# Optimization experiments

Measured on AMD Instinct MI355X. Metric: run time of the kernel, lower is better.

Reference implementation:

```python
import jax, jax.numpy as jnp
import numpy as np

BATCH, N_CHAN, N_FREQ, N_FRAMES = 4, 4, 257, 2000
N_TAPS, N_DELAY, N_ITER = 2, 1, 3
EPS = 1e-3        # eps passed to constructor (used by ISS updates / normalization / proj back)
EPS_MODEL = 1e-5  # eps_models['laplace'] used inside LaplaceModel


def setup_inputs() -> dict:
    key = jax.random.key(0)
    k1, k2 = jax.random.split(key)
    shape = (BATCH, N_CHAN, N_FREQ, N_FRAMES)
    return {
        "X_real": jax.random.normal(k1, shape, dtype=jnp.float32),
        "X_imag": jax.random.normal(k2, shape, dtype=jnp.float32),
    }


def mag_sq(x):
    return jnp.square(x.real) + jnp.square(x.imag)


def divide(num, denom, eps=EPS):
    # torchiva.divide: num / clamp(denom, min=eps); denom is always real here
    return num / jnp.maximum(denom, eps)


def laplace_weights(X):
    # LaplaceModel: 1 / clamp(2*sqrt(sum_f |X|^2), min=eps), broadcast over freq
    denom = 2.0 * jnp.sqrt(jnp.sum(mag_sq(X), axis=-2, keepdims=True))
    return jnp.broadcast_to(1.0 / jnp.maximum(denom, EPS_MODEL), X.shape)


def iss_block_update_type_1(src, X, weights, eps=EPS):
    n_frames = X.shape[-1]
    norm = 1.0 / n_frames
    Xs = X[..., src, :, :]                                            # (..., f, n)
    v_num = jnp.einsum('bcfn,bcfn,bfn->bcf', weights, X, Xs.conj()) * norm
    v_denom = jnp.einsum('bcfn,bfn->bcf', weights, mag_sq(Xs)) * norm
    v = divide(v_num, v_denom, eps)                                   # complex (..., c, f)
    v_s = 1.0 - 1.0 / jnp.sqrt(jnp.maximum(v_denom[..., src, :], eps))
    return v.at[..., src, :].set(v_s.astype(v.dtype))


def iss_block_update_type_2(src, tap, X, X_bar, weights, eps=EPS):
    n_frames = X.shape[-1]
    norm = 1.0 / n_frames
    Xst = X_bar[..., src, :, tap, :]                                  # (..., f, n)
    v_num = jnp.einsum('bcfn,bcfn,bfn->bcf', weights, X, Xst.conj()) * norm
    v_denom = jnp.einsum('bcfn,bfn->bcf', weights, mag_sq(Xst)) * norm
    return divide(v_num, v_denom, eps)


def iss_updates(X, X_bar, W, weights, eps=EPS):
    n_chan = X.shape[-3]
    n_taps = X_bar.shape[-2]
    # sequential rank-1 source updates
    for src in range(n_chan):
        v = iss_block_update_type_1(src, X, weights, eps)
        X = X - jnp.einsum('bcf,bfn->bcfn', v, X[..., src, :, :])
        W = W - jnp.einsum('bcf,bfd->bcfd', v, W[..., src, :, :])
    # sequential rank-1 tap (dereverberation) updates
    for src in range(n_chan):
        for tap in range(n_taps):
            v = iss_block_update_type_2(src, tap, X, X_bar, weights, eps)
            X = X - jnp.einsum('bcf,bfn->bcfn', v, X_bar[..., src, :, tap, :])
    return X, W


def projection_back(Y, W, eps=1e-6):
    n_chan = Y.shape[-3]
    eye = jnp.eye(n_chan, dtype=W.dtype)
    e1 = eye[:, :1]                                                   # ref_mic = 0, shape (c, 1)
    WT = jnp.swapaxes(jnp.swapaxes(W, -3, -2), -2, -1)                # (..., f, d, c)
    a = jnp.linalg.solve(WT + eps * eye, e1)                          # (..., f, c, 1)
    a = jnp.swapaxes(a, -3, -2)                                       # (..., c, f, 1)
    return Y * a


def _forward(X_real, X_imag):
    X = jax.lax.complex(X_real, X_imag)                               # (b, c, f, n)
    batch_shape = X.shape[:-3]
    n_chan, n_freq, n_frames = X.shape[-3:]

    # hankel view of zero-padded signal -> delayed frames X_bar (b, c, f, taps, n)
    P = N_TAPS + N_DELAY
    X_pad = jnp.pad(X, [(0, 0)] * (X.ndim - 1) + [(P, 0)])
    X_bar = jnp.stack([X_pad[..., t:t + n_frames] for t in range(N_TAPS)], axis=-2)

    # demixing filters initialized to identity: W[b, c, f, d] = I[c, d]
    eye = jnp.eye(n_chan, dtype=X.dtype)
    W = jnp.broadcast_to(eye[:, None, :], batch_shape + (n_chan, n_freq, n_chan))

    for _ in range(N_ITER):
        weights = laplace_weights(X)
        g = jnp.maximum(jnp.mean(mag_sq(X), axis=(-2, -1), keepdims=True), EPS)
        g_sqrt = jnp.sqrt(g)
        X = divide(X, g_sqrt, EPS)
        W = divide(W, g_sqrt, EPS)
        weights = weights * g
        X, W = iss_updates(X, X_bar, W, weights, EPS)

    X = projection_back(X, W, eps=EPS)
    # return real/imag stacked so the output is a real float32 array
    return jnp.stack([X.real, X.imag], axis=0)


def reference(X_real, X_imag):
    return _forward(X_real, X_imag)
```

## Files before the change

### kernel.cpp

```cpp
#include <hip/hip_runtime.h>
#include <math.h>

#define NB   4
#define NC   4
#define NF   257
#define NFRM 2000
#define PLANE (NB*NC*NF*NFRM)
#define EPS  1e-3f
#define INV_FN (1.0f/514000.0f)

#define RFC  29
#define RFP  9
#define UT   512
#define UK   4

__device__ __forceinline__ float2 cmulf(float2 a, float2 b) {
  return make_float2(a.x*b.x - a.y*b.y, a.x*b.y + a.y*b.x);
}

#define DPP_STAGE(x, CTRL)                                                \
  x += __int_as_float(__builtin_amdgcn_update_dpp(                        \
        0, __float_as_int(x), CTRL, 0xf, 0xf, true))

__device__ __forceinline__ void wave_reduce12(float* acc) {
  #pragma unroll
  for (int i=0;i<12;i++) {
    float xv = acc[i];
    DPP_STAGE(xv, 0x111);
    DPP_STAGE(xv, 0x112);
    DPP_STAGE(xv, 0x114);
    DPP_STAGE(xv, 0x118);
    DPP_STAGE(xv, 0x142);
    DPP_STAGE(xv, 0x143);
    acc[i] = xv;
  }
}

__global__ __launch_bounds__(256)
void k_zero(float* __restrict__ rsum, float* __restrict__ gpart) {
  int idx = blockIdx.x*256 + threadIdx.x;
  if (idx < 32000) rsum[idx] = 0.f;
  else if (idx < 32048) gpart[idx-32000] = 0.f;
}

__global__ __launch_bounds__(256)
void k_r(const float* __restrict__ Xr, const float* __restrict__ Xi,
         float* __restrict__ rsum, float* __restrict__ gpart)
{
  const int tid = threadIdx.x;
  const int q   = blockIdx.x*256 + tid;
  const int fc  = blockIdx.y;
  const int bc  = blockIdx.z;
  float4 s4 = make_float4(0.f,0.f,0.f,0.f);
  if (q < 500) {
    const int f0 = fc*RFP;
    const int f1 = (f0+RFP < NF) ? (f0+RFP) : NF;
    const float4* r4 = (const float4*)(Xr + (size_t)(bc*NF+f0)*NFRM) + q;
    const float4* i4 = (const float4*)(Xi + (size_t)(bc*NF+f0)*NFRM) + q;
    for (int f=f0; f<f1; ++f) {
      float4 a = *r4, b2 = *i4;
      s4.x += a.x*a.x + b2.x*b2.x;
      s4.y += a.y*a.y + b2.y*b2.y;
      s4.z += a.z*a.z + b2.z*b2.z;
      s4.w += a.w*a.w + b2.w*b2.w;
      r4 += 500; i4 += 500;
    }
    float* rp = rsum + bc*NFRM + q*4;
    atomicAdd(rp+0, s4.x); atomicAdd(rp+1, s4.y);
    atomicAdd(rp+2, s4.z); atomicAdd(rp+3, s4.w);
  }
  float t = s4.x+s4.y+s4.z+s4.w;
  #pragma unroll
  for (int o=32;o;o>>=1) t += __shfl_down(t, o);
  __shared__ float wred[4];
  if ((tid & 63) == 0) wred[tid>>6] = t;
  __syncthreads();
  if (tid == 0) atomicAdd(&gpart[bc], wred[0]+wred[1]+wred[2]+wred[3]);
}

__global__ __launch_bounds__(256)
void k_w(float* __restrict__ rsum, const float* __restrict__ gpart,
         float* __restrict__ w0g)
{
  int idx = blockIdx.x*256 + threadIdx.x;
  int bc  = idx / NFRM;
  float g = fmaxf(gpart[bc]*INV_FN, EPS);
  float r = rsum[idx];
  float s = fmaxf(2.0f*sqrtf(r), 1e-5f);
  w0g[idx] = g * __builtin_amdgcn_rcpf(s);
  rsum[idx] = 0.f;
}

#define REDUCE12()                                                        \
  {                                                                       \
    wave_reduce12(acc);                                                   \
    if ((tid & 63) == 63) {                                               \
      const int wid = tid >> 6;                                           \
      *(float4*)&wpart[wid][0] = make_float4(acc[0],acc[1],acc[2],acc[3]);\
      *(float4*)&wpart[wid][4] = make_float4(acc[4],acc[5],acc[6],acc[7]);\
      *(float4*)&wpart[wid][8] = make_float4(acc[8],acc[9],acc[10],acc[11]);\
    }                                                                     \
    __syncthreads();                                                      \
    if (tid < 12) {                                                       \
      float t = 0.f;                                                      \
      _Pragma("unroll")                                                   \
      for (int w=0;w<8;w++) t += wpart[w][tid];                           \
      vredL[tid] = t;                                                     \
    }                                                                     \
    __syncthreads();                                                      \
    {                                                                     \
      float4 vv0 = *(const float4*)&vredL[0];                             \
      float4 vv1 = *(const float4*)&vredL[4];                             \
      float4 vv2 = *(const float4*)&vredL[8];                             \
      vsum[0]=vv0.x; vsum[1]=vv0.y; vsum[2] =vv0.z; vsum[3] =vv0.w;       \
      vsum[4]=vv1.x; vsum[5]=vv1.y; vsum[6] =vv1.z; vsum[7] =vv1.w;       \
      vsum[8]=vv2.x; vsum[9]=vv2.y; vsum[10]=vv2.z; vsum[11]=vv2.w;       \
    }                                                                     \
  }

template<bool FIRST, bool LAST>
__global__ __launch_bounds__(UT, 2)
void k_u(const float* Xsr, const float* Xsi,
         const float* __restrict__ Xor_, const float* __restrict__ Xoi_,
         float* Xdr, float* Xdi,
         const float* __restrict__ w0gbuf,
         const float* __restrict__ gpart,
         float2* __restrict__ Wg)
{
  __shared__ __align__(16) float wpart[8][16];
  __shared__ __align__(16) float vredL[16];
  __shared__ float2 Wl[NC][NC];
  __shared__ float2 avec[NC];

  const int tid = threadIdx.x;
  const int f = blockIdx.x;
  const int b = blockIdx.y;
  const bool valid = tid < 500;
  const int n0 = tid*UK;
  const float norm = 1.0f/(float)NFRM;

  float igs[NC];
  #pragma unroll
  for (int c=0;c<NC;c++) {
    float g = fmaxf(gpart[b*NC+c]*INV_FN, EPS);
    igs[c] = __builtin_amdgcn_rsqf(g);
  }

  float2 x[NC][UK];
  #pragma unroll
  for (int c=0;c<NC;c++) {
    #pragma unroll
    for (int k=0;k<UK;k++) x[c][k] = make_float2(0.f,0.f);
    if (valid) {
      const size_t rb = ((size_t)(b*NC+c)*NF + f)*NFRM;
      float4 r0 = *(const float4*)(Xsr + rb + n0);
      float4 i0 = *(const float4*)(Xsi + rb + n0);
      x[c][0] = make_float2(r0.x*igs[c], i0.x*igs[c]);
      x[c][1] = make_float2(r0.y*igs[c], i0.y*igs[c]);
      x[c][2] = make_float2(r0.z*igs[c], i0.z*igs[c]);
      x[c][3] = make_float2(r0.w*igs[c], i0.w*igs[c]);
    }
  }
  float w0g[NC][UK];
  #pragma unroll
  for (int c=0;c<NC;c++) {
    #pragma unroll
    for (int k=0;k<UK;k++) w0g[c][k] = 0.f;
    if (valid) {
      float4 w4 = *(const float4*)(w0gbuf + (b*NC+c)*NFRM + n0);
      w0g[c][0]=w4.x; w0g[c][1]=w4.y; w0g[c][2]=w4.z; w0g[c][3]=w4.w;
    }
  }
  if (tid < 16) {
    const int c = tid>>2, d = tid&3;
    float2 w;
    if (FIRST) w = make_float2((c==d)?1.f:0.f, 0.f);
    else       w = Wg[(size_t)(b*NF+f)*16 + tid];
    Wl[c][d] = make_float2(w.x*igs[c], w.y*igs[c]);
  }

  #pragma unroll
  for (int s=0;s<NC;s++) {
    float acc[12];
    #pragma unroll
    for (int i=0;i<12;i++) acc[i] = 0.f;
    #pragma unroll
    for (int k=0;k<UK;k++) {
      float2 xs = x[s][k];
      float m = xs.x*xs.x + xs.y*xs.y;
      #pragma unroll
      for (int c=0;c<NC;c++) {
        float2 xc = x[c][k];
        float w = w0g[c][k];
        acc[c]   += w*(xc.x*xs.x + xc.y*xs.y);
        acc[4+c] += w*(xc.y*xs.x - xc.x*xs.y);
        acc[8+c] += w*m;
      }
    }
    float vsum[12];
    REDUCE12();
    float2 v[NC];
    #pragma unroll
    for (int c=0;c<NC;c++) {
      float dn = fmaxf(vsum[8+c]*norm, EPS);
      float rc = __builtin_amdgcn_rcpf(dn) * norm;
      v[c] = make_float2(vsum[c]*rc, vsum[4+c]*rc);
    }
    v[s] = make_float2(1.0f - __builtin_amdgcn_rsqf(fmaxf(vsum[8+s]*norm, EPS)), 0.f);
    #pragma unroll
    for (int k=0;k<UK;k++) {
      float2 xs = x[s][k];
      #pragma unroll
      for (int c=0;c<NC;c++) {
        float2 xv = x[c][k];
        xv.x -= v[c].x*xs.x - v[c].y*xs.y;
        xv.y -= v[c].x*xs.y + v[c].y*xs.x;
        x[c][k] = xv;
      }
    }
    if (tid < 16) {
      const int c = tid>>2, d = tid&3;
      float2 wsd = Wl[s][d];
      float2 wv = Wl[c][d];
      wv.x -= v[c].x*wsd.x - v[c].y*wsd.y;
      wv.y -= v[c].x*wsd.y + v[c].y*wsd.x;
      Wl[c][d] = wv;
    }
  }

  float winr[8], wini[8], nxtr[8], nxti[8];
  {
    const size_t ob = ((size_t)(b*NC+0)*NF + f)*NFRM;
    float4 m1r=make_float4(0,0,0,0), m1i=m1r, p0r=m1r, p0i=m1r;
    if (valid) {
      const float* tp = Xor_ + ob + n0;
      const float* ti = Xoi_ + ob + n0;
      if (tid > 0) { m1r = *(const float4*)(tp-4); m1i = *(const float4*)(ti-4); }
      p0r = *(const float4*)tp;  p0i = *(const float4*)ti;
    }
    winr[0]=m1r.x; winr[1]=m1r.y; winr[2]=m1r.z; winr[3]=m1r.w;
    winr[4]=p0r.x; winr[5]=p0r.y; winr[6]=p0r.z; winr[7]=p0r.w;
    wini[0]=m1i.x; wini[1]=m1i.y; wini[2]=m1i.z; wini[3]=m1i.w;
    wini[4]=p0i.x; wini[5]=p0i.y; wini[6]=p0i.z; wini[7]=p0i.w;
  }
  #pragma unroll 1
  for (int s=0;s<NC;s++) {
    if (s < NC-1) {
      const size_t ob = ((size_t)(b*NC+s+1)*NF + f)*NFRM;
      float4 m1r=make_float4(0,0,0,0), m1i=m1r, p0r=m1r, p0i=m1r;
      if (valid) {
        const float* tp = Xor_ + ob + n0;
        const float* ti = Xoi_ + ob + n0;
        if (tid > 0) { m1r = *(const float4*)(tp-4); m1i = *(const float4*)(ti-4); }
        p0r = *(const float4*)tp;  p0i = *(const float4*)ti;
      }
      nxtr[0]=m1r.x; nxtr[1]=m1r.y; nxtr[2]=m1r.z; nxtr[3]=m1r.w;
      nxtr[4]=p0r.x; nxtr[5]=p0r.y; nxtr[6]=p0r.z; nxtr[7]=p0r.w;
      nxti[0]=m1i.x; nxti[1]=m1i.y; nxti[2]=m1i.z; nxti[3]=m1i.w;
      nxti[4]=p0i.x; nxti[5]=p0i.y; nxti[6]=p0i.z; nxti[7]=p0i.w;
    }
    #pragma unroll
    for (int t2=0;t2<2;t2++) {
      float acc[12];
      #pragma unroll
      for (int i=0;i<12;i++) acc[i] = 0.f;
      #pragma unroll
      for (int k=0;k<UK;k++) {
        float2 xs = make_float2(winr[k+1+t2], wini[k+1+t2]);
        float m = xs.x*xs.x + xs.y*xs.y;
        #pragma unroll
        for (int c=0;c<NC;c++) {
          float2 xc = x[c][k];
          float w = w0g[c][k];
          acc[c]   += w*(xc.x*xs.x + xc.y*xs.y);
          acc[4+c] += w*(xc.y*xs.x - xc.x*xs.y);
          acc[8+c] += w*m;
        }
      }
      float vsum[12];
      REDUCE12();
      float2 v[NC];
      #pragma unroll
      for (int c=0;c<NC;c++) {
        float dn = fmaxf(vsum[8+c]*norm, EPS);
        float rc = __builtin_amdgcn_rcpf(dn) * norm;
        v[c] = make_float2(vsum[c]*rc, vsum[4+c]*rc);
      }
      #pragma unroll
      for (int k=0;k<UK;k++) {
        float2 xs = make_float2(winr[k+1+t2], wini[k+1+t2]);
        #pragma unroll
        for (int c=0;c<NC;c++) {
          float2 xv = x[c][k];
          xv.x -= v[c].x*xs.x - v[c].y*xs.y;
          xv.y -= v[c].x*xs.y + v[c].y*xs.x;
          x[c][k] = xv;
        }
      }
    }
    #pragma unroll
    for (int j=0;j<8;j++) { winr[j]=nxtr[j]; wini[j]=nxti[j]; }
  }

  if (LAST) {
    if (tid == 0) {
      float2 A[4][4], bb[4], xv[4];
      for (int i=0;i<4;i++)
        for (int j=0;j<4;j++)
          A[i][j] = Wl[j][i];
      for (int i=0;i<4;i++) A[i][i].x += 1e-6f;
      bb[0] = make_float2(1.f,0.f);
      bb[1] = make_float2(0.f,0.f);
      bb[2] = make_float2(0.f,0.f);
      bb[3] = make_float2(0.f,0.f);
      for (int col=0; col<4; ++col) {
        int p = col;
        float best = A[col][col].x*A[col][col].x + A[col][col].y*A[col][col].y;
        for (int r=col+1;r<4;r++) {
          float m = A[r][col].x*A[r][col].x + A[r][col].y*A[r][col].y;
          if (m > best) { best = m; p = r; }
        }
        if (p != col) {
          for (int j=0;j<4;j++) { float2 ts = A[col][j]; A[col][j] = A[p][j]; A[p][j] = ts; }
          float2 ts = bb[col]; bb[col] = bb[p]; bb[p] = ts;
        }
        float2 piv = A[col][col];
        float ib = 1.0f / (piv.x*piv.x + piv.y*piv.y);
        float2 inv = make_float2(piv.x*ib, -piv.y*ib);
        for (int r=col+1;r<4;r++) {
          float2 fac = cmulf(A[r][col], inv);
          for (int j=col;j<4;j++) {
            float2 pr = cmulf(fac, A[col][j]);
            A[r][j].x -= pr.x; A[r][j].y -= pr.y;
          }
          float2 pb = cmulf(fac, bb[col]);
          bb[r].x -= pb.x; bb[r].y -= pb.y;
        }
      }
      for (int r=3;r>=0;r--) {
        float2 t = bb[r];
        for (int j=r+1;j<4;j++) {
          float2 pr = cmulf(A[r][j], xv[j]);
          t.x -= pr.x; t.y -= pr.y;
        }
        float2 d = A[r][r];
        float ib = 1.0f/(d.x*d.x + d.y*d.y);
        xv[r] = cmulf(t, make_float2(d.x*ib, -d.y*ib));
      }
      for (int c=0;c<4;c++) avec[c] = xv[c];
    }
    __syncthreads();
    if (valid) {
      #pragma unroll
      for (int c=0;c<NC;c++) {
        const size_t rb = ((size_t)(b*NC+c)*NF + f)*NFRM;
        float2 a = avec[c];
        float2 y0 = cmulf(a, x[c][0]), y1 = cmulf(a, x[c][1]);
        float2 y2 = cmulf(a, x[c][2]), y3 = cmulf(a, x[c][3]);
        *(float4*)(Xdr + rb + n0) = make_float4(y0.x,y1.x,y2.x,y3.x);
        *(float4*)(Xdi + rb + n0) = make_float4(y0.y,y1.y,y2.y,y3.y);
      }
    }
  } else {
    if (valid) {
      #pragma unroll
      for (int c=0;c<NC;c++) {
        const size_t rb = ((size_t)(b*NC+c)*NF + f)*NFRM;
        *(float4*)(Xdr + rb + n0) = make_float4(x[c][0].x,x[c][1].x,x[c][2].x,x[c][3].x);
        *(float4*)(Xdi + rb + n0) = make_float4(x[c][0].y,x[c][1].y,x[c][2].y,x[c][3].y);
      }
    }
    if (tid < 16) Wg[(size_t)(b*NF+f)*16 + tid] = Wl[tid>>2][tid&3];
  }
}

extern "C" void kernel_launch(void* const* d_in, const int* in_sizes, int n_in,
                              void* d_out, int out_size, void* d_ws, size_t ws_size,
                              hipStream_t stream)
{
  (void)in_sizes; (void)n_in; (void)out_size; (void)ws_size;
  const float* xr_in = (const float*)d_in[0];
  const float* xi_in = (const float*)d_in[1];
  float* outr = (float*)d_out;
  float* outi = outr + PLANE;

  char*  ws    = (char*)d_ws;
  float* rsum  = (float*)ws;
  float* w0g   = (float*)(ws + 128000);
  float* gpart = (float*)(ws + 256000);
  float2* Wg   = (float2*)(ws + 256000 + 256);

  dim3 grR(2, RFC, NB*NC);
  dim3 grU(NF, NB);

  k_zero<<<126, 256, 0, stream>>>(rsum, gpart);

  k_r<<<grR, 256, 0, stream>>>(xr_in, xi_in, rsum, gpart + 0);
  k_w<<<125, 256, 0, stream>>>(rsum, gpart + 0, w0g);
  k_u<true,false><<<grU, UT, 0, stream>>>(xr_in, xi_in, xr_in, xi_in,
                                          outr, outi, w0g, gpart + 0, Wg);
  k_r<<<grR, 256, 0, stream>>>(outr, outi, rsum, gpart + 16);
  k_w<<<125, 256, 0, stream>>>(rsum, gpart + 16, w0g);
  k_u<false,false><<<grU, UT, 0, stream>>>(outr, outi, xr_in, xi_in,
                                           outr, outi, w0g, gpart + 16, Wg);
  k_r<<<grR, 256, 0, stream>>>(outr, outi, rsum, gpart + 32);
  k_w<<<125, 256, 0, stream>>>(rsum, gpart + 32, w0g);
  k_u<false,true><<<grU, UT, 0, stream>>>(outr, outi, xr_in, xi_in,
                                          outr, outi, w0g, gpart + 32, Wg);
}
```

Baseline: 541.6 us.

## Pair consecutive ISS rank-1 updates to halve block reductions

Pairs consecutive sequential rank-1 updates (two type-1 sources, and both delay taps of each type-2 source). Extra cross-term statistics are accumulated so the second update's coefficients can be derived algebraically from the first without a second block-wide reduction. This halves the number of reductions and __syncthreads barriers per block, but each reduction now carries 32 values instead of 12, which raises register pressure. The prefetch of the next source's delayed frames is dropped in favour of loading inside the loop.

```diff
diff --git a/kernel.cpp b/kernel.cpp
--- a/kernel.cpp
+++ b/kernel.cpp
@@ -22,9 +22,10 @@
   x += __int_as_float(__builtin_amdgcn_update_dpp(                        \
         0, __float_as_int(x), CTRL, 0xf, 0xf, true))
 
-__device__ __forceinline__ void wave_reduce12(float* acc) {
-  #pragma unroll
-  for (int i=0;i<12;i++) {
+template<int N>
+__device__ __forceinline__ void wave_reduceN(float* acc) {
+  #pragma unroll
+  for (int i=0;i<N;i++) {
     float xv = acc[i];
     DPP_STAGE(xv, 0x111);
     DPP_STAGE(xv, 0x112);
@@ -91,30 +92,28 @@
   rsum[idx] = 0.f;
 }
 
-#define REDUCE12()                                                        \
+#define REDUCE32()                                                        \
   {                                                                       \
-    wave_reduce12(acc);                                                   \
+    wave_reduceN<32>(acc);                                                \
     if ((tid & 63) == 63) {                                               \
       const int wid = tid >> 6;                                           \
-      *(float4*)&wpart[wid][0] = make_float4(acc[0],acc[1],acc[2],acc[3]);\
-      *(float4*)&wpart[wid][4] = make_float4(acc[4],acc[5],acc[6],acc[7]);\
-      *(float4*)&wpart[wid][8] = make_float4(acc[8],acc[9],acc[10],acc[11]);\
+      _Pragma("unroll")                                                   \
+      for (int j=0;j<8;j++)                                               \
+        *(float4*)&wpart[wid][j*4] =                                      \
+          make_float4(acc[j*4],acc[j*4+1],acc[j*4+2],acc[j*4+3]);         \
     }                                                                     \
     __syncthreads();                                                      \
-    if (tid < 12) {                                                       \
+    if (tid < 32) {                                                       \
       float t = 0.f;                                                      \
       _Pragma("unroll")                                                   \
       for (int w=0;w<8;w++) t += wpart[w][tid];                           \
       vredL[tid] = t;                                                     \
     }                                                                     \
     __syncthreads();                                                      \
-    {                                                                     \
-      float4 vv0 = *(const float4*)&vredL[0];                             \
-      float4 vv1 = *(const float4*)&vredL[4];                             \
-      float4 vv2 = *(const float4*)&vredL[8];                             \
-      vsum[0]=vv0.x; vsum[1]=vv0.y; vsum[2] =vv0.z; vsum[3] =vv0.w;       \
-      vsum[4]=vv1.x; vsum[5]=vv1.y; vsum[6] =vv1.z; vsum[7] =vv1.w;       \
-      vsum[8]=vv2.x; vsum[9]=vv2.y; vsum[10]=vv2.z; vsum[11]=vv2.w;       \
+    _Pragma("unroll")                                                     \
+    for (int j=0;j<8;j++) {                                               \
+      float4 vv = *(const float4*)&vredL[j*4];                            \
+      vsum[j*4]=vv.x; vsum[j*4+1]=vv.y; vsum[j*4+2]=vv.z; vsum[j*4+3]=vv.w; \
     }                                                                     \
   }
 
@@ -127,8 +126,8 @@
          const float* __restrict__ gpart,
          float2* __restrict__ Wg)
 {
-  __shared__ __align__(16) float wpart[8][16];
-  __shared__ __align__(16) float vredL[16];
+  __shared__ __align__(16) float wpart[8][32];
+  __shared__ __align__(16) float vredL[32];
   __shared__ float2 Wl[NC][NC];
   __shared__ float2 avec[NC];
 
@@ -180,73 +179,97 @@
   }
 
   #pragma unroll
-  for (int s=0;s<NC;s++) {
-    float acc[12];
-    #pragma unroll
-    for (int i=0;i<12;i++) acc[i] = 0.f;
+  for (int p=0;p<2;p++) {
+    const int sg = 2*p, tu = 2*p+1;
+    float acc[32];
+    #pragma unroll
+    for (int i=0;i<32;i++) acc[i] = 0.f;
     #pragma unroll
     for (int k=0;k<UK;k++) {
-      float2 xs = x[s][k];
-      float m = xs.x*xs.x + xs.y*xs.y;
-      #pragma unroll
-      for (int c=0;c<NC;c++) {
-        float2 xc = x[c][k];
-        float w = w0g[c][k];
-        acc[c]   += w*(xc.x*xs.x + xc.y*xs.y);
-        acc[4+c] += w*(xc.y*xs.x - xc.x*xs.y);
-        acc[8+c] += w*m;
-      }
-    }
-    float vsum[12];
-    REDUCE12();
-    float2 v[NC];
+      float2 xs = x[sg][k], xt = x[tu][k];
+      float m00 = xs.x*xs.x + xs.y*xs.y;
+      float m11 = xt.x*xt.x + xt.y*xt.y;
+      float prx = xs.x*xt.x + xs.y*xt.y;
+      float pry = xs.y*xt.x - xs.x*xt.y;
+      #pragma unroll
+      for (int c=0;c<NC;c++) {
+        float w = w0g[c][k]; float2 xc = x[c][k];
+        acc[c]    += w*(xc.x*xs.x + xc.y*xs.y);
+        acc[4+c]  += w*(xc.y*xs.x - xc.x*xs.y);
+        acc[8+c]  += w*(xc.x*xt.x + xc.y*xt.y);
+        acc[12+c] += w*(xc.y*xt.x - xc.x*xt.y);
+        acc[16+c] += w*m00;
+        acc[20+c] += w*m11;
+        acc[24+c] += w*prx;
+        acc[28+c] += w*pry;
+      }
+    }
+    float vsum[32];
+    REDUCE32();
+    float2 v0[NC], v1[NC];
     #pragma unroll
     for (int c=0;c<NC;c++) {
-      float dn = fmaxf(vsum[8+c]*norm, EPS);
-      float rc = __builtin_amdgcn_rcpf(dn) * norm;
-      v[c] = make_float2(vsum[c]*rc, vsum[4+c]*rc);
-    }
-    v[s] = make_float2(1.0f - __builtin_amdgcn_rsqf(fmaxf(vsum[8+s]*norm, EPS)), 0.f);
+      float dn = fmaxf(vsum[16+c]*norm, EPS);
+      float rc = __builtin_amdgcn_rcpf(dn)*norm;
+      v0[c] = make_float2(vsum[c]*rc, vsum[4+c]*rc);
+    }
+    v0[sg] = make_float2(1.0f - __builtin_amdgcn_rsqf(fmaxf(vsum[16+sg]*norm, EPS)), 0.f);
+    const float2 v0t = v0[tu];
+    float d1t = 0.f;
+    #pragma unroll
+    for (int c=0;c<NC;c++) {
+      float2 A = make_float2(vsum[c],    vsum[4+c]);
+      float2 B = make_float2(vsum[8+c],  vsum[12+c]);
+      float  Pp = vsum[16+c], Qq = vsum[20+c];
+      float2 S = make_float2(vsum[24+c], vsum[28+c]);
+      float2 ca = make_float2(v0t.x*A.x + v0t.y*A.y, v0t.x*A.y - v0t.y*A.x);
+      float2 vc = v0[c];
+      float2 vs = cmulf(vc, S);
+      float2 vv = make_float2(vc.x*v0t.x + vc.y*v0t.y, vc.y*v0t.x - vc.x*v0t.y);
+      float2 n1 = make_float2(B.x - ca.x - vs.x + vv.x*Pp,
+                              B.y - ca.y - vs.y + vv.y*Pp);
+      float d1 = Qq - 2.f*(v0t.x*S.x - v0t.y*S.y) + (v0t.x*v0t.x + v0t.y*v0t.y)*Pp;
+      if (c == tu) d1t = d1;
+      float dn = fmaxf(d1*norm, EPS);
+      float rc = __builtin_amdgcn_rcpf(dn)*norm;
+      v1[c] = make_float2(n1.x*rc, n1.y*rc);
+    }
+    v1[tu] = make_float2(1.0f - __builtin_amdgcn_rsqf(fmaxf(d1t*norm, EPS)), 0.f);
     #pragma unroll
     for (int k=0;k<UK;k++) {
-      float2 xs = x[s][k];
-      #pragma unroll
-      for (int c=0;c<NC;c++) {
-        float2 xv = x[c][k];
-        xv.x -= v[c].x*xs.x - v[c].y*xs.y;
-        xv.y -= v[c].x*xs.y + v[c].y*xs.x;
-        x[c][k] = xv;
+      float2 xs = x[sg][k];
+      #pragma unroll
+      for (int c=0;c<NC;c++) {
+        float2 pr = cmulf(v0[c], xs);
+        x[c][k].x -= pr.x; x[c][k].y -= pr.y;
+      }
+      float2 xt = x[tu][k];
+      #pragma unroll
+      for (int c=0;c<NC;c++) {
+        float2 pr = cmulf(v1[c], xt);
+        x[c][k].x -= pr.x; x[c][k].y -= pr.y;
       }
     }
     if (tid < 16) {
       const int c = tid>>2, d = tid&3;
-      float2 wsd = Wl[s][d];
+      float2 ws0 = Wl[sg][d];
+      float2 pr0 = cmulf(v0[c], ws0);
       float2 wv = Wl[c][d];
-      wv.x -= v[c].x*wsd.x - v[c].y*wsd.y;
-      wv.y -= v[c].x*wsd.y + v[c].y*wsd.x;
+      wv.x -= pr0.x; wv.y -= pr0.y;
       Wl[c][d] = wv;
-    }
-  }
-
-  float winr[8], wini[8], nxtr[8], nxti[8];
-  {
-    const size_t ob = ((size_t)(b*NC+0)*NF + f)*NFRM;
-    float4 m1r=make_float4(0,0,0,0), m1i=m1r, p0r=m1r, p0i=m1r;
-    if (valid) {
-      const float* tp = Xor_ + ob + n0;
-      const float* ti = Xoi_ + ob + n0;
-      if (tid > 0) { m1r = *(const float4*)(tp-4); m1i = *(const float4*)(ti-4); }
-      p0r = *(const float4*)tp;  p0i = *(const float4*)ti;
-    }
-    winr[0]=m1r.x; winr[1]=m1r.y; winr[2]=m1r.z; winr[3]=m1r.w;
-    winr[4]=p0r.x; winr[5]=p0r.y; winr[6]=p0r.z; winr[7]=p0r.w;
-    wini[0]=m1i.x; wini[1]=m1i.y; wini[2]=m1i.z; wini[3]=m1i.w;
-    wini[4]=p0i.x; wini[5]=p0i.y; wini[6]=p0i.z; wini[7]=p0i.w;
-  }
+      float2 ws1 = Wl[tu][d];
+      float2 pr1 = cmulf(v1[c], ws1);
+      wv = Wl[c][d];
+      wv.x -= pr1.x; wv.y -= pr1.y;
+      Wl[c][d] = wv;
+    }
+  }
+
   #pragma unroll 1
   for (int s=0;s<NC;s++) {
-    if (s < NC-1) {
-      const size_t ob = ((size_t)(b*NC+s+1)*NF + f)*NFRM;
+    const size_t ob = ((size_t)(b*NC+s)*NF + f)*NFRM;
+    float winr[8], wini[8];
+    {
       float4 m1r=make_float4(0,0,0,0), m1i=m1r, p0r=m1r, p0i=m1r;
       if (valid) {
         const float* tp = Xor_ + ob + n0;
@@ -254,52 +277,62 @@
         if (tid > 0) { m1r = *(const float4*)(tp-4); m1i = *(const float4*)(ti-4); }
         p0r = *(const float4*)tp;  p0i = *(const float4*)ti;
       }
-      nxtr[0]=m1r.x; nxtr[1]=m1r.y; nxtr[2]=m1r.z; nxtr[3]=m1r.w;
-      nxtr[4]=p0r.x; nxtr[5]=p0r.y; nxtr[6]=p0r.z; nxtr[7]=p0r.w;
-      nxti[0]=m1i.x; nxti[1]=m1i.y; nxti[2]=m1i.z; nxti[3]=m1i.w;
-      nxti[4]=p0i.x; nxti[5]=p0i.y; nxti[6]=p0i.z; nxti[7]=p0i.w;
-    }
-    #pragma unroll
-    for (int t2=0;t2<2;t2++) {
-      float acc[12];
-      #pragma unroll
-      for (int i=0;i<12;i++) acc[i] = 0.f;
-      #pragma unroll
-      for (int k=0;k<UK;k++) {
-        float2 xs = make_float2(winr[k+1+t2], wini[k+1+t2]);
-        float m = xs.x*xs.x + xs.y*xs.y;
-        #pragma unroll
-        for (int c=0;c<NC;c++) {
-          float2 xc = x[c][k];
-          float w = w0g[c][k];
-          acc[c]   += w*(xc.x*xs.x + xc.y*xs.y);
-          acc[4+c] += w*(xc.y*xs.x - xc.x*xs.y);
-          acc[8+c] += w*m;
-        }
-      }
-      float vsum[12];
-      REDUCE12();
-      float2 v[NC];
-      #pragma unroll
-      for (int c=0;c<NC;c++) {
-        float dn = fmaxf(vsum[8+c]*norm, EPS);
-        float rc = __builtin_amdgcn_rcpf(dn) * norm;
-        v[c] = make_float2(vsum[c]*rc, vsum[4+c]*rc);
-      }
-      #pragma unroll
-      for (int k=0;k<UK;k++) {
-        float2 xs = make_float2(winr[k+1+t2], wini[k+1+t2]);
-        #pragma unroll
-        for (int c=0;c<NC;c++) {
-          float2 xv = x[c][k];
-          xv.x -= v[c].x*xs.x - v[c].y*xs.y;
-          xv.y -= v[c].x*xs.y + v[c].y*xs.x;
-          x[c][k] = xv;
-        }
-      }
-    }
-    #pragma unroll
-    for (int j=0;j<8;j++) { winr[j]=nxtr[j]; wini[j]=nxti[j]; }
+      winr[0]=m1r.x; winr[1]=m1r.y; winr[2]=m1r.z; winr[3]=m1r.w;
+      winr[4]=p0r.x; winr[5]=p0r.y; winr[6]=p0r.z; winr[7]=p0r.w;
+      wini[0]=m1i.x; wini[1]=m1i.y; wini[2]=m1i.z; wini[3]=m1i.w;
+      wini[4]=p0i.x; wini[5]=p0i.y; wini[6]=p0i.z; wini[7]=p0i.w;
+    }
+    float acc[32];
+    #pragma unroll
+    for (int i=0;i<32;i++) acc[i] = 0.f;
+    #pragma unroll
+    for (int k=0;k<UK;k++) {
+      float2 u0 = make_float2(winr[k+1], wini[k+1]);
+      float2 u1 = make_float2(winr[k+2], wini[k+2]);
+      float m0 = u0.x*u0.x + u0.y*u0.y;
+      float m1 = u1.x*u1.x + u1.y*u1.y;
+      float crx = u0.x*u1.x + u0.y*u1.y;
+      float cry = u0.y*u1.x - u0.x*u1.y;
+      #pragma unroll
+      for (int c=0;c<NC;c++) {
+        float w = w0g[c][k]; float2 xc = x[c][k];
+        acc[c]    += w*(xc.x*u0.x + xc.y*u0.y);
+        acc[4+c]  += w*(xc.y*u0.x - xc.x*u0.y);
+        acc[8+c]  += w*(xc.x*u1.x + xc.y*u1.y);
+        acc[12+c] += w*(xc.y*u1.x - xc.x*u1.y);
+        acc[16+c] += w*m0;
+        acc[20+c] += w*m1;
+        acc[24+c] += w*crx;
+        acc[28+c] += w*cry;
+      }
+    }
+    float vsum[32];
+    REDUCE32();
+    float2 v0[NC], v1[NC];
+    #pragma unroll
+    for (int c=0;c<NC;c++) {
+      float dn0 = fmaxf(vsum[16+c]*norm, EPS);
+      float rc0 = __builtin_amdgcn_rcpf(dn0)*norm;
+      v0[c] = make_float2(vsum[c]*rc0, vsum[4+c]*rc0);
+      float2 C = make_float2(vsum[24+c], vsum[28+c]);
+      float2 n1 = make_float2(vsum[8+c]  - (v0[c].x*C.x - v0[c].y*C.y),
+                              vsum[12+c] - (v0[c].x*C.y + v0[c].y*C.x));
+      float dn1 = fmaxf(vsum[20+c]*norm, EPS);
+      float rc1 = __builtin_amdgcn_rcpf(dn1)*norm;
+      v1[c] = make_float2(n1.x*rc1, n1.y*rc1);
+    }
+    #pragma unroll
+    for (int k=0;k<UK;k++) {
+      float2 u0 = make_float2(winr[k+1], wini[k+1]);
+      float2 u1 = make_float2(winr[k+2], wini[k+2]);
+      #pragma unroll
+      for (int c=0;c<NC;c++) {
+        float2 p0 = cmulf(v0[c], u0);
+        float2 p1 = cmulf(v1[c], u1);
+        x[c][k].x -= p0.x + p1.x;
+        x[c][k].y -= p0.y + p1.y;
+      }
+    }
   }
 
   if (LAST) {
```

Result: no change. 542.8 us (+0.2%).
